# Kernel optimization log

Measured on AMD Instinct MI355X. Metric: run time of the kernel, lower is better.

The kernel has to match this reference:

```python
import jax, jax.numpy as jnp
import numpy as np

V, D, L, H, FF, B, S = 32000, 2048, 4, 16, 8192, 2, 2048
DH = D // H
PRUNE_LAYERS = (1, 2)   # layers with an attached pruning module
KEEP_RATIO = 0.5        # keep_ratio arg of forward_prefill_with_pruning


def _rms(x, w, eps=1e-6):
    return x * w * jax.lax.rsqrt(jnp.mean(x * x, -1, keepdims=True) + eps)


def _rope(x):
    # x: [B,H,s,DH]; position_ids = arange(s), recomputed after every pruning step
    s = x.shape[2]
    half = DH // 2
    inv = 1.0 / (10000.0 ** (jnp.arange(half, dtype=jnp.float32) / half))
    ang = jnp.arange(s, dtype=jnp.float32)[:, None] * inv  # [s, half]
    cos, sin = jnp.cos(ang), jnp.sin(ang)
    x1, x2 = x[..., :half], x[..., half:]
    return jnp.concatenate([x1 * cos - x2 * sin, x1 * sin + x2 * cos], -1)


def _block(h, mask, wq, wk, wv, wo, wg, wu, wd, ln1, ln2):
    b, s, _ = h.shape
    hn = _rms(h, ln1)
    q = _rope((hn @ wq).reshape(b, s, H, DH).transpose(0, 2, 1, 3))
    k = _rope((hn @ wk).reshape(b, s, H, DH).transpose(0, 2, 1, 3))
    v = (hn @ wv).reshape(b, s, H, DH).transpose(0, 2, 1, 3)
    att = jnp.einsum('bhqd,bhkd->bhqk', q, k) / np.float32(np.sqrt(DH))
    allowed = jnp.tril(jnp.ones((s, s), bool)) & (mask[:, None, None, :] > 0)
    att = jnp.where(allowed, att, jnp.float32(-1e9))
    o = jnp.einsum('bhqk,bhkd->bhqd', jax.nn.softmax(att, -1), v)
    h = h + o.transpose(0, 2, 1, 3).reshape(b, s, D) @ wo
    hn = _rms(h, ln2)
    h = h + (jax.nn.silu(hn @ wg) * (hn @ wu)) @ wd
    return h


def _forward(input_ids, attention_mask, embed, wq, wk, wv, wo, wg, wu, wd, ln1, ln2, lnf, lm_head, scorer):
    h = embed[input_ids]        # [B,S,D]
    mask = attention_mask
    for i in range(L):
        if i in PRUNE_LAYERS:
            pi = PRUNE_LAYERS.index(i)
            # pruning module: Linear(D->2); keep score = logits[..., 0]
            sc = jnp.einsum('bsd,cd->bsc', h, scorer[pi])[..., 0]
            kk = max(1, int(h.shape[1] * KEEP_RATIO))      # static under jit
            _, idx = jax.lax.top_k(sc, kk)
            idx = jnp.sort(idx, -1)                        # sorted kept indices
            h = jnp.take_along_axis(h, idx[..., None], axis=1)
            mask = jnp.take_along_axis(mask, idx, axis=1)
        h = _block(h, mask, wq[i], wk[i], wv[i], wo[i], wg[i], wu[i], wd[i], ln1[i], ln2[i])
    return _rms(h, lnf) @ lm_head   # logits [B, S_pruned, V]


def setup_inputs() -> dict:
    key = jax.random.key(0)
    ks = jax.random.split(key, 12)
    g = lambda k, shape: jax.random.normal(k, shape, jnp.float32) * 0.02
    return {
        'input_ids': jax.random.randint(ks[0], (B, S), 0, V, jnp.int32),
        'attention_mask': jnp.ones((B, S), jnp.int32),
        'embed': g(ks[1], (V, D)),
        'wq': g(ks[2], (L, D, D)),
        'wk': g(ks[3], (L, D, D)),
        'wv': g(ks[4], (L, D, D)),
        'wo': g(ks[5], (L, D, D)),
        'wg': g(ks[6], (L, D, FF)),
        'wu': g(ks[7], (L, D, FF)),
        'wd': g(ks[8], (L, FF, D)),
        'ln1': jnp.ones((L, D), jnp.float32),
        'ln2': jnp.ones((L, D), jnp.float32),
        'lnf': jnp.ones((D,), jnp.float32),
        'lm_head': g(ks[9], (D, V)),
        'scorer': g(ks[10], (len(PRUNE_LAYERS), 2, D)),
    }


def reference(input_ids, attention_mask, embed, wq, wk, wv, wo, wg, wu, wd, ln1, ln2, lnf, lm_head, scorer):
    return _forward(input_ids, attention_mask, embed, wq, wk, wv, wo, wg, wu, wd, ln1, ln2, lnf, lm_head, scorer)
```

## Files before the change

### kernel.cpp

```cpp
#include <hip/hip_runtime.h>
#include <math.h>


#define DD 2048
#define HH 16
#define DHH 128
#define FFF 8192
#define BBATCH 2
#define SSEQ 2048
#define VV 32000
#define LLAYERS 4

typedef float4 f4;
typedef __attribute__((ext_vector_type(8))) short short8;
typedef __attribute__((ext_vector_type(4))) float f32x4;
typedef unsigned short u16;

__device__ inline u16 bf16rne(float x) {
    unsigned u = __float_as_uint(x);
    unsigned r = (u + 0x7FFFu + ((u >> 16) & 1u)) >> 16;
    return (u16)r;
}
__device__ inline float bf16tof(u16 h) {
    return __uint_as_float(((unsigned)h) << 16);
}

__device__ __forceinline__ void gload16(const u16* g, u16* l) {
    __builtin_amdgcn_global_load_lds(
        (const __attribute__((address_space(1))) unsigned int*)g,
        (__attribute__((address_space(3))) unsigned int*)l, 16, 0, 0);
}

#define BARRIER() do { asm volatile("" ::: "memory"); \
    __builtin_amdgcn_s_barrier(); asm volatile("" ::: "memory"); } while (0)

__device__ __forceinline__ void xcd_swz(int& bx, int& by) {
    int gx = gridDim.x;
    int nwg = gx * gridDim.y;
    int orig = by * gx + bx;
    int q = nwg >> 3, r = nwg & 7;
    int xcd = orig & 7, loc = orig >> 3;
    int swz = (xcd < r ? xcd * (q + 1) : r * (q + 1) + (xcd - r) * q) + loc;
    bx = swz % gx;
    by = swz / gx;
}

__global__ void k_embed(const int* __restrict__ ids, const float* __restrict__ emb,
                        float* __restrict__ out) {
    int row = blockIdx.x;
    int id  = ids[row];
    const f4* src = (const f4*)(emb + (size_t)id * DD);
    f4*       dst = (f4*)(out + (size_t)row * DD);
    for (int i = threadIdx.x; i < DD / 4; i += blockDim.x) dst[i] = src[i];
}

__global__ void k_copy_int(const int* __restrict__ src, int* __restrict__ dst, int n) {
    int i = blockIdx.x * blockDim.x + threadIdx.x;
    if (i < n) dst[i] = src[i];
}

__global__ void k_addN(float* __restrict__ H, const float* __restrict__ P,
                       long len, int nparts) {
    long i = (long)blockIdx.x * 256 + threadIdx.x;
    if (i >= len / 4) return;
    f4 h = ((f4*)H)[i];
    for (int z = 0; z < nparts; z++) {
        f4 p = ((const f4*)(P + (size_t)z * len))[i];
        h.x += p.x; h.y += p.y; h.z += p.z; h.w += p.w;
    }
    ((f4*)H)[i] = h;
}

__global__ __launch_bounds__(256) void k_rmsnorm_cvt(const float* __restrict__ x,
                                                     const float* __restrict__ w,
                                                     u16* __restrict__ OH,
                                                     u16* __restrict__ OL) {
    int row = blockIdx.x;
    const float* xr = x + (size_t)row * DD;
    float ss = 0.f;
    for (int i = threadIdx.x; i < DD / 4; i += blockDim.x) {
        f4 v = ((const f4*)xr)[i];
        ss += v.x * v.x + v.y * v.y + v.z * v.z + v.w * v.w;
    }
    for (int o = 32; o > 0; o >>= 1) ss += __shfl_down(ss, o);
    __shared__ float red[4];
    int wid = threadIdx.x >> 6, lane = threadIdx.x & 63;
    if (lane == 0) red[wid] = ss;
    __syncthreads();
    float tot = red[0] + red[1] + red[2] + red[3];
    float inv = 1.0f / sqrtf(tot / (float)DD + 1e-6f);
    for (int i = threadIdx.x; i < DD / 4; i += blockDim.x) {
        f4 v = ((const f4*)xr)[i];
        f4 wv = ((const f4*)w)[i];
        float o[4];
        o[0] = v.x * wv.x * inv; o[1] = v.y * wv.y * inv;
        o[2] = v.z * wv.z * inv; o[3] = v.w * wv.w * inv;
        ushort4 hv, lv;
        u16* hp = (u16*)&hv; u16* lp = (u16*)&lv;
#pragma unroll
        for (int j = 0; j < 4; j++) {
            u16 h = bf16rne(o[j]);
            hp[j] = h;
            lp[j] = bf16rne(o[j] - bf16tof(h));
        }
        *(ushort4*)&OH[(size_t)row * DD + i * 4] = hv;
        *(ushort4*)&OL[(size_t)row * DD + i * 4] = lv;
    }
}

__global__ __launch_bounds__(256) void k_cvt_w(const float* __restrict__ W,
                                               u16* __restrict__ WtH,
                                               u16* __restrict__ WtL,
                                               int K, int N, int nc0, int dn0,
                                               int writeLo) {
    __shared__ float T[64][65];
    int tid = threadIdx.x;
    int n0g = nc0 + blockIdx.x * 64;
    int k0  = blockIdx.y * 64;
#pragma unroll
    for (int it = 0; it < 4; it++) {
        int r = it * 16 + (tid >> 4);
        int c4 = (tid & 15) * 4;
        f4 v = *(const f4*)(W + (size_t)(k0 + r) * N + n0g + c4);
        T[r][c4 + 0] = v.x; T[r][c4 + 1] = v.y;
        T[r][c4 + 2] = v.z; T[r][c4 + 3] = v.w;
    }
    __syncthreads();
    int nl = tid >> 2;
    int ks = (tid & 3) * 16;
    u16 hi[16], lo[16];
#pragma unroll
    for (int j = 0; j < 16; j++) {
        float v = T[ks + j][nl];
        u16 h = bf16rne(v);
        hi[j] = h;
        lo[j] = bf16rne(v - bf16tof(h));
    }
    size_t base = (size_t)(dn0 + blockIdx.x * 64 + nl) * K + k0 + ks;
    *(short8*)&WtH[base]     = *(short8*)&hi[0];
    *(short8*)&WtH[base + 8] = *(short8*)&hi[8];
    if (writeLo) {
        *(short8*)&WtL[base]     = *(short8*)&lo[0];
        *(short8*)&WtL[base + 8] = *(short8*)&lo[8];
    }
}

template <int PASSES, int RES, int DUAL>
__global__ __launch_bounds__(256, 2) void k_bgemm(const u16* __restrict__ AH,
                                                  const u16* __restrict__ AL,
                                                  const u16* __restrict__ B1H,
                                                  const u16* __restrict__ B1L,
                                                  const u16* __restrict__ B2H,
                                                  const u16* __restrict__ B2L,
                                                  const float* __restrict__ Rsrc,
                                                  float* __restrict__ C,
                                                  u16* __restrict__ OH,
                                                  u16* __restrict__ OL,
                                                  int M, int ldC, int K) {
    constexpr int NW = DUAL ? 2 : 1;
    __shared__ u16 As[128 * 32];
    __shared__ u16 Bs[NW][128 * 32];
    int tid = threadIdx.x;
    int bx = blockIdx.x, by = blockIdx.y;
    xcd_swz(bx, by);
    int m0 = by * 128, n0 = bx * 128;
    int lane = tid & 63, w = tid >> 6;
    int wm = w >> 1, wn = w & 1;
    int lr = lane & 15, lq = lane >> 4;
    int grow = lane >> 2;
    int gcol = (lane & 3) * 8;

    f32x4 acc[NW][4][4];
#pragma unroll
    for (int u = 0; u < NW; u++)
#pragma unroll
        for (int i = 0; i < 4; i++)
#pragma unroll
            for (int j = 0; j < 4; j++)
#pragma unroll
                for (int r = 0; r < 4; r++) acc[u][i][j][r] = 0.f;

    const int KT = PASSES * K;
    for (int kb = 0; kb < KT; kb += 32) {
        int p  = (PASSES > 1) ? ((kb >= 2 * K) ? 2 : ((kb >= K) ? 1 : 0)) : 0;
        int ks = kb - p * K;
        const u16* Ab = ((p == 2) ? AL  : AH)  + (size_t)(m0 + w * 32) * K + ks;
        const u16* Bb = ((p == 1) ? B1L : B1H) + (size_t)(n0 + w * 32) * K + ks;
        __syncthreads();
        gload16(Ab + (size_t)grow * K + gcol,        &As[w * 1024]);
        gload16(Ab + (size_t)(grow + 16) * K + gcol, &As[w * 1024 + 512]);
        gload16(Bb + (size_t)grow * K + gcol,        &Bs[0][w * 1024]);
        gload16(Bb + (size_t)(grow + 16) * K + gcol, &Bs[0][w * 1024 + 512]);
        if constexpr (DUAL) {
            const u16* B2b = ((p == 1) ? B2L : B2H) + (size_t)(n0 + w * 32) * K + ks;
            gload16(B2b + (size_t)grow * K + gcol,        &Bs[1][w * 1024]);
            gload16(B2b + (size_t)(grow + 16) * K + gcol, &Bs[1][w * 1024 + 512]);
        }
// ... 184 lines not shown
    }

#pragma unroll
    for (int i16 = 0; i16 < 8; i16++) {
#pragma unroll
        for (int jj = 0; jj < 4; jj++) {
            int gm = m0 + (i16 >> 2) * 128 + wm * 64 + (i16 & 3) * 16 + lq * 4;
            int gn = n0 + (jj >> 1) * 128 + wn * 32 + (jj & 1) * 16 + lr;
#pragma unroll
            for (int r = 0; r < 4; r++) {
                size_t off = (size_t)(gm + r) * ldC + gn;
                float v = acc[i16][jj][r];
                if constexpr (PLANE) {
                    u16 h = bf16rne(v);
                    OH[off] = h;
                    OL[off] = bf16rne(v - bf16tof(h));
                } else {
                    C[off] = v;
                }
            }
        }
    }
}

__global__ __launch_bounds__(256) void k_silu_cvt(const u16* __restrict__ Gh,
                                                  const u16* __restrict__ Gl,
                                                  u16* __restrict__ FH,
                                                  u16* __restrict__ FL, long n8) {
    long i = (long)blockIdx.x * 256 + threadIdx.x;
    if (i >= n8) return;
    short8 gh = ((const short8*)Gh)[i], gl = ((const short8*)Gl)[i];
    short8 uh = ((const short8*)FH)[i], ul = ((const short8*)FL)[i];
    short8 oh, ol;
#pragma unroll
    for (int e = 0; e < 8; e++) {
        float g = bf16tof((u16)gh[e]) + bf16tof((u16)gl[e]);
        float u = bf16tof((u16)uh[e]) + bf16tof((u16)ul[e]);
        float v = g / (1.0f + expf(-g)) * u;
        u16 h = bf16rne(v);
        oh[e] = (short)h;
        ol[e] = (short)bf16rne(v - bf16tof(h));
    }
    ((short8*)FH)[i] = oh;
    ((short8*)FL)[i] = ol;
}

__global__ void k_rope_table(float* __restrict__ cosT, float* __restrict__ sinT) {
    int idx = blockIdx.x * blockDim.x + threadIdx.x;
    if (idx >= SSEQ * 64) return;
    int pos = idx >> 6, d = idx & 63;
    float p   = (float)pow(10000.0, (double)d * (1.0 / 64.0));
    float inv = 1.0f / p;
    float ang = (float)pos * inv;
    cosT[idx] = (float)cos((double)ang);
    sinT[idx] = (float)sin((double)ang);
}

__global__ void k_rope(float* __restrict__ C,
                       const float* __restrict__ cosT, const float* __restrict__ sinT,
                       int s, int ld) {
    int bi = blockIdx.x;
    int h = bi % HH;
    int i = (bi / HH) % s;
    size_t base = (size_t)(bi / HH) * ld + h * DHH;
    int d = threadIdx.x;
    float c  = cosT[i * 64 + d];
    float sn = sinT[i * 64 + d];
    float x1 = C[base + d], x2 = C[base + 64 + d];
    C[base + d]      = x1 * c - x2 * sn;
    C[base + 64 + d] = x1 * sn + x2 * c;
    x1 = C[base + 2048 + d]; x2 = C[base + 2048 + 64 + d];
    C[base + 2048 + d]      = x1 * c - x2 * sn;
    C[base + 2048 + 64 + d] = x1 * sn + x2 * c;
}

__global__ __launch_bounds__(256) void k_cvt_qk(const float* __restrict__ C,
                                                u16* __restrict__ QHp, u16* __restrict__ QLp,
                                                u16* __restrict__ KHp, u16* __restrict__ KLp) {
    int row = blockIdx.x;
    int c = threadIdx.x * 8;
#pragma unroll
    for (int sec = 0; sec < 2; sec++) {
        const float* src = C + (size_t)row * 6144 + sec * 2048 + c;
        u16* dh = (sec ? KHp : QHp) + (size_t)row * 2048 + c;
        u16* dl = (sec ? KLp : QLp) + (size_t)row * 2048 + c;
        u16 hbuf[8], lbuf[8];
#pragma unroll
        for (int q = 0; q < 2; q++) {
            f4 v = *(const f4*)(src + q * 4);
            float a[4] = {v.x, v.y, v.z, v.w};
#pragma unroll
            for (int e = 0; e < 4; e++) {
                u16 h = bf16rne(a[e]);
                hbuf[q * 4 + e] = h;
                lbuf[q * 4 + e] = bf16rne(a[e] - bf16tof(h));
            }
        }
        *(short8*)dh = *(short8*)&hbuf[0];
        *(short8*)dl = *(short8*)&lbuf[0];
    }
}

__global__ __launch_bounds__(256) void k_cvt_vt(const float* __restrict__ C,
                                                u16* __restrict__ VtH,
                                                u16* __restrict__ VtL, int s) {
    __shared__ float T[64][132];
    int bh = blockIdx.y;
    int h = bh & 15, b = bh >> 4;
    int kv0 = blockIdx.x * 64;
    int t = threadIdx.x;
#pragma unroll
    for (int it = 0; it < 8; it++) {
        int kv = it * 8 + (t >> 5);
        int c4 = (t & 31) * 4;
        f4 v = *(const f4*)(C + (size_t)((size_t)b * s + kv0 + kv) * 6144 + 4096 + h * 128 + c4);
        T[kv][c4 + 0] = v.x; T[kv][c4 + 1] = v.y;
        T[kv][c4 + 2] = v.z; T[kv][c4 + 3] = v.w;
    }
    __syncthreads();
    int d = t >> 1, seg = t & 1;
    size_t base = ((size_t)bh * 128 + d) * s + kv0 + seg * 32;
#pragma unroll
    for (int g = 0; g < 4; g++) {
        u16 h8[8], l8[8];
#pragma unroll
        for (int e = 0; e < 8; e++) {
            float v = T[seg * 32 + g * 8 + e][d];
            u16 hh = bf16rne(v);
            h8[e] = hh;
            l8[e] = bf16rne(v - bf16tof(hh));
        }
        int gp = (g ^ ((d >> 1) & 3)) * 8;
        *(short8*)&VtH[base + gp] = *(short8*)&h8[0];
        *(short8*)&VtL[base + gp] = *(short8*)&l8[0];
    }
}

template <int PASSES>
__global__ __launch_bounds__(256, 2) void k_attn_mfma(
        const u16* __restrict__ QHp, const u16* __restrict__ QLp,
        const u16* __restrict__ KHp, const u16* __restrict__ KLp,
        const u16* __restrict__ VtH, const u16* __restrict__ VtL,
        const int* __restrict__ mask,
        u16* __restrict__ OH, u16* __restrict__ OL, int s) {
    constexpr int BUFU = (PASSES > 1) ? 16384 : 8192;
    constexpr int VOFF = (PASSES > 1) ? 8192 : 4096;
    __shared__ u16 SM[2 * BUFU + 5120];
    int tid = threadIdx.x, lane = tid & 63, w = tid >> 6;
    int lr = lane & 15, lq = lane >> 4;
    int grow = lane >> 2;
    int sgcol = (((lane & 3) ^ ((lane >> 3) & 3))) * 8;
    int gcol  = (lane & 3) * 8;
    int rc = (lq ^ ((lr >> 1) & 3)) * 8;
    int qt = gridDim.x - 1 - blockIdx.x;
    int bh = blockIdx.y;
    int h = bh & 15, b = bh >> 4;
    int q0 = qt * 64;
    size_t rb = (size_t)b * s;
    const u16* vtH = VtH + (size_t)bh * 128 * s;
    const u16* vtL = VtL + (size_t)bh * 128 * s;
    u16* PHw = SM + 2 * BUFU + w * 1280;
    u16* PLw = PHw + 640;
    const float scale = 0.08838834764831845f;

    short8 qh[4], ql[4];
    {
        const u16* qp = QHp + (rb + q0) * 2048 + h * 128 + w * 32;
#pragma unroll
        for (int it = 0; it < 4; it++)
            gload16(qp + (size_t)(it * 16 + grow) * 2048 + sgcol, SM + w * 2048 + it * 512);
        __syncthreads();
#pragma unroll
        for (int ks = 0; ks < 4; ks++)
            qh[ks] = *(const short8*)&SM[ks * 2048 + (w * 16 + lr) * 32 + rc];
        if constexpr (PASSES > 1) {
            __syncthreads();
            const u16* qp2 = QLp + (rb + q0) * 2048 + h * 128 + w * 32;
#pragma unroll
            for (int it = 0; it < 4; it++)
                gload16(qp2 + (size_t)(it * 16 + grow) * 2048 + sgcol, SM + w * 2048 + it * 512);
            __syncthreads();
#pragma unroll
            for (int ks = 0; ks < 4; ks++)
                ql[ks] = *(const short8*)&SM[ks * 2048 + (w * 16 + lr) * 32 + rc];
        }
        __syncthreads();
    }

    auto kv_stage = [&](int t, int buf) {
        u16* base = SM + buf * BUFU;
        const u16* kp = KHp + (rb + t * 32) * 2048 + h * 128 + w * 32;
        gload16(kp + (size_t)grow * 2048 + sgcol,        base + w * 1024);
        gload16(kp + (size_t)(16 + grow) * 2048 + sgcol, base + w * 1024 + 512);
        const u16* vp = vtH + (size_t)(w * 32) * s + t * 32;
        gload16(vp + (size_t)grow * s + gcol,        base + VOFF + (w * 32) * 32);
        gload16(vp + (size_t)(16 + grow) * s + gcol, base + VOFF + (w * 32 + 16) * 32);
        if constexpr (PASSES > 1) {
            const u16* kp2 = KLp + (rb + t * 32) * 2048 + h * 128 + w * 32;
            gload16(kp2 + (size_t)grow * 2048 + sgcol,        base + 4096 + w * 1024);
            gload16(kp2 + (size_t)(16 + grow) * 2048 + sgcol, base + 4096 + w * 1024 + 512);
            const u16* vp2 = vtL + (size_t)(w * 32) * s + t * 32;
            gload16(vp2 + (size_t)grow * s + gcol,        base + 12288 + (w * 32) * 32);
            gload16(vp2 + (size_t)(16 + grow) * s + gcol, base + 12288 + (w * 32 + 16) * 32);
        }
    };

    f32x4 o_acc[8];
#pragma unroll
    for (int j = 0; j < 8; j++)
#pragma unroll
        for (int r = 0; r < 4; r++) o_acc[j][r] = 0.f;
    float m_run[4], l_run[4];
#pragma unroll
    for (int r = 0; r < 4; r++) { m_run[r] = -3.0e38f; l_run[r] = 0.f; }

    int nt = (q0 + 64) >> 5;
    int mv0 = mask[rb + lr];
    int mv1 = mask[rb + 16 + lr];
    kv_stage(0, 0);
    for (int t = 0; t < nt; t++) {
        int bsel = t & 1;
        if (t + 1 < nt) {
            kv_stage(t + 1, 1 - bsel);
            if constexpr (PASSES > 1)
                asm volatile("s_waitcnt vmcnt(8)" ::: "memory");
            else
                asm volatile("s_waitcnt vmcnt(4)" ::: "memory");
        } else {
            asm volatile("s_waitcnt vmcnt(0)" ::: "memory");
        }
        BARRIER();
        int nmv0 = mv0, nmv1 = mv1;
        if (t + 1 < nt) {
            nmv0 = mask[rb + (t + 1) * 32 + lr];
            nmv1 = mask[rb + (t + 1) * 32 + 16 + lr];
        }
        const u16* KsH = SM + bsel * BUFU;
        const u16* KsL = KsH + 4096;
        const u16* VsH = SM + bsel * BUFU + VOFF;
        const u16* VsL = SM + bsel * BUFU + 12288;
        f32x4 sa[2];
#pragma unroll
        for (int j = 0; j < 2; j++)
#pragma unroll
            for (int r = 0; r < 4; r++) sa[j][r] = 0.f;
#pragma unroll
        for (int j = 0; j < 2; j++) {
#pragma unroll
            for (int ks = 0; ks < 4; ks++) {
                short8 kb = *(const short8*)&KsH[ks * 1024 + (j * 16 + lr) * 32 + rc];
                sa[j] = __builtin_amdgcn_mfma_f32_16x16x32_bf16(qh[ks], kb, sa[j], 0, 0, 0);
                if constexpr (PASSES > 1) {
                    short8 kl2 = *(const short8*)&KsL[ks * 1024 + (j * 16 + lr) * 32 + rc];
                    sa[j] = __builtin_amdgcn_mfma_f32_16x16x32_bf16(qh[ks], kl2, sa[j], 0, 0, 0);
                    sa[j] = __builtin_amdgcn_mfma_f32_16x16x32_bf16(ql[ks], kb, sa[j], 0, 0, 0);
                }
            }
        }
        float sclv[4];
#pragma unroll
        for (int r = 0; r < 4; r++) {
            int ig = q0 + w * 16 + lq * 4 + r;
            float v0 = (t * 32 + lr <= ig && mv0 > 0) ? sa[0][r] * scale : -1.0e9f;
            float v1 = (t * 32 + 16 + lr <= ig && mv1 > 0) ? sa[1][r] * scale : -1.0e9f;
            float mx = fmaxf(v0, v1);
            mx = fmaxf(mx, __shfl_xor(mx, 1));
            mx = fmaxf(mx, __shfl_xor(mx, 2));
            mx = fmaxf(mx, __shfl_xor(mx, 4));
            mx = fmaxf(mx, __shfl_xor(mx, 8));
            float mo = m_run[r];
            float mn = fmaxf(mo, mx);
            float p0 = expf(v0 - mn), p1 = expf(v1 - mn);
            float ps = p0 + p1;
            ps += __shfl_xor(ps, 1);
            ps += __shfl_xor(ps, 2);
            ps += __shfl_xor(ps, 4);
            ps += __shfl_xor(ps, 8);
            sclv[r] = expf(mo - mn);
            m_run[r] = mn;
            l_run[r] = l_run[r] * sclv[r] + ps;
            int prow = lq * 4 + r;
            u16 h0 = bf16rne(p0);
            u16 h1 = bf16rne(p1);
            PHw[prow * 40 + lr] = h0;
            PHw[prow * 40 + 16 + lr] = h1;
            if constexpr (PASSES > 1) {
                PLw[prow * 40 + lr] = bf16rne(p0 - bf16tof(h0));
                PLw[prow * 40 + 16 + lr] = bf16rne(p1 - bf16tof(h1));
            }
        }
#pragma unroll
        for (int j = 0; j < 8; j++)
#pragma unroll
            for (int r = 0; r < 4; r++) o_acc[j][r] *= sclv[r];
        short8 ph = *(const short8*)&PHw[lr * 40 + lq * 8];
        short8 pl;
        if constexpr (PASSES > 1) pl = *(const short8*)&PLw[lr * 40 + lq * 8];
#pragma unroll
        for (int j = 0; j < 8; j++) {
            int vrow = j * 16 + lr;
            short8 vh = *(const short8*)&VsH[vrow * 32 + rc];
            o_acc[j] = __builtin_amdgcn_mfma_f32_16x16x32_bf16(ph, vh, o_acc[j], 0, 0, 0);
            if constexpr (PASSES > 1) {
                short8 vl = *(const short8*)&VsL[vrow * 32 + rc];
                o_acc[j] = __builtin_amdgcn_mfma_f32_16x16x32_bf16(ph, vl, o_acc[j], 0, 0, 0);
                o_acc[j] = __builtin_amdgcn_mfma_f32_16x16x32_bf16(pl, vh, o_acc[j], 0, 0, 0);
            }
        }
        BARRIER();
        mv0 = nmv0; mv1 = nmv1;
    }
#pragma unroll
    for (int r = 0; r < 4; r++) {
        float linv = 1.0f / l_run[r];
        size_t rowoff = (rb + q0 + w * 16 + lq * 4 + r) * 2048 + h * 128 + lr;
#pragma unroll
        for (int j = 0; j < 8; j++) {
            float v = o_acc[j][r] * linv;
            u16 hh = bf16rne(v);
            OH[rowoff + j * 16] = hh;
            OL[rowoff + j * 16] = bf16rne(v - bf16tof(hh));
        }
    }
}

__global__ __launch_bounds__(256, 2) void k_attn_f32(const float* __restrict__ Q,
                                                     const float* __restrict__ K,
                                                     const float* __restrict__ V,
                                                     const int* __restrict__ mask,
                                                     u16* __restrict__ OH,
                                                     u16* __restrict__ OL, int s, int ld) {
    int qt = blockIdx.x, bh = blockIdx.y;
    int h = bh & (HH - 1), b = bh >> 4;
    __shared__ float Qs[64][132];
    __shared__ float Ks[32 * 128];
    __shared__ float Vs[32][132];
    __shared__ float Ps[64][36];
    __shared__ float mrow[64], lrow[64];
    int tid = threadIdx.x;
    int tx = tid & 15, ty = tid >> 4;

#pragma unroll
    for (int p = 0; p < 2; p++) {
        int r = p * 32 + (tid >> 3);
        int kb = (tid & 7) * 4;
        const float* src = Q + (size_t)(b * s + qt * 64 + r) * ld + h * DHH;
#pragma unroll
        for (int q = 0; q < 4; q++)
            *(f4*)&Qs[r][kb + 32 * q] = *(const f4*)(src + kb + 32 * q);
    }
    if (tid < 64) { mrow[tid] = -3.0e38f; lrow[tid] = 0.f; }

    float acc[4][8];
#pragma unroll
    for (int i = 0; i < 4; i++)
#pragma unroll
        for (int c = 0; c < 8; c++) acc[i][c] = 0.f;
    const float scale = 0.08838834764831845f;

    int ktmax = 2 * (qt + 1);
    for (int kt = 0; kt < ktmax; kt++) {
        __syncthreads();
#pragma unroll
        for (int p = 0; p < 4; p++) {
            int c = p * 8 + (tid >> 5);
            int kk = (tid & 31) * 4;
            size_t g = (size_t)(b * s + kt * 32 + c) * ld + h * DHH + kk;
            f4 kv = *(const f4*)(K + g);
            int ch = (kk >> 2) ^ (c >> 1);
            *(f4*)&Ks[c * 128 + ch * 4] = kv;
            *(f4*)&Vs[c][kk] = *(const f4*)(V + g);
        }
        __syncthreads();
        float sv[4][2];
#pragma unroll
        for (int i = 0; i < 4; i++) { sv[i][0] = 0.f; sv[i][1] = 0.f; }
        for (int kk = 0; kk < 128; kk += 4) {
            f4 qv[4];
#pragma unroll
            for (int i = 0; i < 4; i++) qv[i] = *(const f4*)&Qs[ty * 4 + i][kk];
#pragma unroll
            for (int j = 0; j < 2; j++) {
                int c = tx * 2 + j;
                int ch = (kk >> 2) ^ (c >> 1);
                f4 kv = *(const f4*)&Ks[c * 128 + ch * 4];
#pragma unroll
                for (int i = 0; i < 4; i++)
                    sv[i][j] += qv[i].x * kv.x + qv[i].y * kv.y +
                                qv[i].z * kv.z + qv[i].w * kv.w;
            }
        }
        float scl[4];
#pragma unroll
        for (int i = 0; i < 4; i++) {
            int r = ty * 4 + i;
            int igl = qt * 64 + r;
#pragma unroll
            for (int j = 0; j < 2; j++) {
                int jg = kt * 32 + tx * 2 + j;
                bool ok = (jg <= igl) && (mask[b * s + jg] > 0);
                sv[i][j] = ok ? sv[i][j] * scale : -1.0e9f;
            }
            float rmax = fmaxf(sv[i][0], sv[i][1]);
            rmax = fmaxf(rmax, __shfl_xor(rmax, 1));
            rmax = fmaxf(rmax, __shfl_xor(rmax, 2));
            rmax = fmaxf(rmax, __shfl_xor(rmax, 4));
            rmax = fmaxf(rmax, __shfl_xor(rmax, 8));
            float mold = mrow[r];
            float mnew = fmaxf(mold, rmax);
            float p0 = expf(sv[i][0] - mnew);
            float p1 = expf(sv[i][1] - mnew);
            float ps = p0 + p1;
            ps += __shfl_xor(ps, 1);
            ps += __shfl_xor(ps, 2);
            ps += __shfl_xor(ps, 4);
            ps += __shfl_xor(ps, 8);
            scl[i] = expf(mold - mnew);
            if (tx == 0) { mrow[r] = mnew; lrow[r] = lrow[r] * scl[i] + ps; }
            float2 pw; pw.x = p0; pw.y = p1;
            *(float2*)&Ps[r][tx * 2] = pw;
        }
        __syncthreads();
#pragma unroll
        for (int i = 0; i < 4; i++) {
            float sc = scl[i];
#pragma unroll
            for (int c = 0; c < 8; c++) acc[i][c] *= sc;
        }
        for (int jj = 0; jj < 32; jj += 4) {
            f4 pv[4];
#pragma unroll
            for (int i = 0; i < 4; i++) pv[i] = *(const f4*)&Ps[ty * 4 + i][jj];
#pragma unroll
            for (int j2 = 0; j2 < 4; j2++) {
                f4 va = *(const f4*)&Vs[jj + j2][tx * 4];
                f4 vb = *(const f4*)&Vs[jj + j2][64 + tx * 4];
#pragma unroll
                for (int i = 0; i < 4; i++) {
                    float p = (&pv[i].x)[j2];
                    acc[i][0] += p * va.x; acc[i][1] += p * va.y;
                    acc[i][2] += p * va.z; acc[i][3] += p * va.w;
                    acc[i][4] += p * vb.x; acc[i][5] += p * vb.y;
                    acc[i][6] += p * vb.z; acc[i][7] += p * vb.w;
                }
            }
        }
    }
    __syncthreads();
#pragma unroll
    for (int i = 0; i < 4; i++) {
        int r = ty * 4 + i;
        float linv = 1.0f / lrow[r];
        size_t ob = (size_t)(b * s + qt * 64 + r) * DD + h * DHH;
        ushort4 h1, l1, h2, l2;
        u16 *h1p = (u16*)&h1, *l1p = (u16*)&l1, *h2p = (u16*)&h2, *l2p = (u16*)&l2;
#pragma unroll
        for (int c = 0; c < 4; c++) {
            float v = acc[i][c] * linv;
            u16 hh = bf16rne(v);
            h1p[c] = hh; l1p[c] = bf16rne(v - bf16tof(hh));
            float v2 = acc[i][c + 4] * linv;
            u16 hh2 = bf16rne(v2);
            h2p[c] = hh2; l2p[c] = bf16rne(v2 - bf16tof(hh2));
        }
        *(ushort4*)&OH[ob + tx * 4] = h1;
        *(ushort4*)&OL[ob + tx * 4] = l1;
        *(ushort4*)&OH[ob + 64 + tx * 4] = h2;
        *(ushort4*)&OL[ob + 64 + tx * 4] = l2;
    }
}

__global__ __launch_bounds__(256) void k_score(const float* __restrict__ Hb,
                                               const float* __restrict__ srow,
                                               float* __restrict__ sc) {
// ... 41 lines not shown
}

__global__ void k_gather(const float* __restrict__ Hin, const int* __restrict__ idx,
                         float* __restrict__ Hout, int s, int kk) {
    int row = blockIdx.x;
    int b = row / kk, p = row % kk;
    int i = idx[b * kk + p];
    const f4* src = (const f4*)(Hin + (size_t)(b * s + i) * DD);
    f4* dst = (f4*)(Hout + (size_t)row * DD);
    for (int t = threadIdx.x; t < DD / 4; t += blockDim.x) dst[t] = src[t];
}

__global__ void k_gather_mask(const int* __restrict__ Min, const int* __restrict__ idx,
                              int* __restrict__ Mout, int s, int kk) {
    int t = blockIdx.x * blockDim.x + threadIdx.x;
    if (t < BBATCH * kk) {
        int b = t / kk, p = t % kk;
        Mout[t] = Min[b * s + idx[b * kk + p]];
    }
}

extern "C" void kernel_launch(void* const* d_in, const int* in_sizes, int n_in,
                              void* d_out, int out_size, void* d_ws, size_t ws_size,
                              hipStream_t stream) {
    const int*   input_ids = (const int*)d_in[0];
    const int*   attn_mask = (const int*)d_in[1];
    const float* embed     = (const float*)d_in[2];
    const float* wq        = (const float*)d_in[3];
    const float* wk        = (const float*)d_in[4];
    const float* wv        = (const float*)d_in[5];
    const float* wo        = (const float*)d_in[6];
    const float* wg        = (const float*)d_in[7];
    const float* wu        = (const float*)d_in[8];
    const float* wd        = (const float*)d_in[9];
    const float* ln1       = (const float*)d_in[10];
    const float* ln2       = (const float*)d_in[11];
    const float* lnf       = (const float*)d_in[12];
    const float* lm_head   = (const float*)d_in[13];
    const float* scorer    = (const float*)d_in[14];

    float* ws = (float*)d_ws;
    const size_t R = (size_t)BBATCH * SSEQ * DD;
    const size_t MISC_FLOATS = 2 * SSEQ * 64 + 5 * (size_t)BBATCH * SSEQ + 1024;
    const size_t NEED_A = (14 * R + MISC_FLOATS) * 4;
    const bool bigws = (ws_size >= NEED_A);

    float* H0   = ws;
    float* H1   = ws + R;
    float* CQKV = ws + 2 * R;
    u16*   AH   = (u16*)(ws + 5 * R);
    u16*   AL   = AH + (size_t)4096 * DD;

    u16* QHp = (u16*)(ws + 6 * R);
    u16* QLp = QHp + (size_t)4096 * DD;
    u16* KHp = (u16*)(ws + 7 * R);
    u16* KLp = KHp + (size_t)4096 * DD;
    u16* VtH = (u16*)(ws + 8 * R);
    u16* VtL = VtH + (size_t)4096 * DD;
    u16* FH  = (u16*)(ws + 6 * R);
    u16* FL  = (u16*)(ws + 8 * R);
    u16* WH1 = (u16*)(ws + 10 * R);
    u16* WL1 = WH1 + (size_t)FFF * DD;
    u16* WH2 = (u16*)(ws + 12 * R);
    u16* WL2 = WH2 + (size_t)FFF * DD;
    u16* WDH = (u16*)(ws + 10 * R);
    u16* WDL = WDH + (size_t)DD * FFF;
    u16* WQKVH = (u16*)(ws + 10 * R);
    u16* WQKVL = WQKVH + (size_t)6144 * DD;

    u16* cWgH = (u16*)CQKV;
    u16* cWgL = cWgH + (size_t)2048 * DD;
    u16* cWuH = cWgL + (size_t)2048 * DD;
    u16* cWuL = cWuH + (size_t)2048 * DD;
    u16* cFH  = (u16*)(ws + 3 * R);
    u16* cFL  = cFH + (size_t)4096 * 2048;
    u16* cWdH = (u16*)(ws + 4 * R);
    u16* cWdL = cWdH + (size_t)2048 * DD;

    float* miscB = ws + (bigws ? 14 * R : 6 * R);
    float* COS = miscB;
    float* SIN = COS + SSEQ * 64;
    float* SC  = SIN + SSEQ * 64;
    int*   FLG = (int*)(SC + (size_t)BBATCH * SSEQ);
    int*   IDX = FLG + BBATCH * SSEQ;
    int*   M0  = IDX + BBATCH * SSEQ;
    int*   M1  = M0 + BBATCH * SSEQ;

    k_rope_table<<<(SSEQ * 64 + 255) / 256, 256, 0, stream>>>(COS, SIN);
    k_embed<<<BBATCH * SSEQ, 256, 0, stream>>>(input_ids, embed, H0);
    k_copy_int<<<(BBATCH * SSEQ + 255) / 256, 256, 0, stream>>>(attn_mask, M0, BBATCH * SSEQ);

    float* Hc = H0; float* Nc = H1;
    int*   Mc = M0; int*   Mt = M1;
    int s = SSEQ;

    for (int l = 0; l < LLAYERS; l++) {
        if (l == 1 || l == 2) {
            int pi = l - 1;
            int kk = s / 2;
            k_score<<<BBATCH * s, 256, 0, stream>>>(Hc, scorer + (size_t)pi * 2 * DD, SC);
            k_rank<<<BBATCH * s, 256, 0, stream>>>(SC, FLG, s, kk);
            k_compact<<<BBATCH, 64, 0, stream>>>(FLG, IDX, s, kk);
            k_gather<<<BBATCH * kk, 256, 0, stream>>>(Hc, IDX, Nc, s, kk);
            k_gather_mask<<<(BBATCH * kk + 255) / 256, 256, 0, stream>>>(Mc, IDX, Mt, s, kk);
            { float* t = Hc; Hc = Nc; Nc = t; }
            { int* t = Mc; Mc = Mt; Mt = t; }
            s = kk;
        }
        int rows = BBATCH * s;
        const bool hiP = (l < 2);
        const int wlo = hiP ? 1 : 0;
        const float* Wq = wq + (size_t)l * DD * DD;
        const float* Wk = wk + (size_t)l * DD * DD;
        const float* Wv = wv + (size_t)l * DD * DD;
        const float* Wo = wo + (size_t)l * DD * DD;
        const float* Wg = wg + (size_t)l * DD * FFF;
        const float* Wu = wu + (size_t)l * DD * FFF;
        const float* Wd = wd + (size_t)l * FFF * DD;
        const float* L1 = ln1 + (size_t)l * DD;
        const float* L2 = ln2 + (size_t)l * DD;

        dim3 gWd(DD / 64, DD / 64);

        k_rmsnorm_cvt<<<rows, 256, 0, stream>>>(Hc, L1, AH, AL);
        if (bigws) {
            k_cvt_w<<<gWd, 256, 0, stream>>>(Wq, WQKVH, WQKVL, DD, DD, 0, 0, wlo);
            k_cvt_w<<<gWd, 256, 0, stream>>>(Wk, WQKVH, WQKVL, DD, DD, 0, 2048, wlo);
            k_cvt_w<<<gWd, 256, 0, stream>>>(Wv, WQKVH, WQKVL, DD, DD, 0, 4096, wlo);
            if (rows >= 2048) {
                dim3 gQKV(6144 / 256, rows / 256);
                if (hiP) k_bg256<3,0><<<gQKV,512,0,stream>>>(AH,AL,WQKVH,WQKVL,CQKV,nullptr,nullptr,rows,6144,DD,DD);
                else     k_bg256<1,0><<<gQKV,512,0,stream>>>(AH,AL,WQKVH,WQKVL,CQKV,nullptr,nullptr,rows,6144,DD,DD);
            } else {
                dim3 gQKV(6144 / 128, rows / 128);
                k_bgemm<1,0,0><<<gQKV,256,0,stream>>>(AH,AL,WQKVH,WQKVL,nullptr,nullptr,nullptr,CQKV,nullptr,nullptr,rows,6144,DD);
            }
        } else {
            u16* WtH = (u16*)Nc;
            u16* WtL = WtH + (size_t)DD * DD;
            dim3 gG(DD / 128, rows / 128);
            const float* Wqkv[3] = {Wq, Wk, Wv};
            for (int q3 = 0; q3 < 3; q3++) {
                k_cvt_w<<<gWd, 256, 0, stream>>>(Wqkv[q3], WtH, WtL, DD, DD, 0, 0, wlo);
                float* Cb = CQKV + q3 * 2048;
                if (hiP) k_bgemm<3,0,0><<<gG,256,0,stream>>>(AH,AL,WtH,WtL,nullptr,nullptr,nullptr,Cb,nullptr,nullptr,rows,6144,DD);
                else     k_bgemm<1,0,0><<<gG,256,0,stream>>>(AH,AL,WtH,WtL,nullptr,nullptr,nullptr,Cb,nullptr,nullptr,rows,6144,DD);
            }
        }
        k_rope<<<rows * HH, 64, 0, stream>>>(CQKV, COS, SIN, s, 6144);

        if (bigws) {
            k_cvt_qk<<<rows, 256, 0, stream>>>(CQKV, QHp, QLp, KHp, KLp);
            k_cvt_vt<<<dim3(s / 64, BBATCH * HH), 256, 0, stream>>>(CQKV, VtH, VtL, s);
            if (hiP) k_attn_mfma<3><<<dim3(s / 64, BBATCH * HH), 256, 0, stream>>>(
                         QHp, QLp, KHp, KLp, VtH, VtL, Mc, AH, AL, s);
            else     k_attn_mfma<1><<<dim3(s / 64, BBATCH * HH), 256, 0, stream>>>(
                         QHp, QLp, KHp, KLp, VtH, VtL, Mc, AH, AL, s);
        } else {
            k_attn_f32<<<dim3(s / 64, BBATCH * HH), 256, 0, stream>>>(
                CQKV, CQKV + 2048, CQKV + 4096, Mc, AH, AL, s, 6144);
        }

        {
            u16* WtH = bigws ? WQKVH : (u16*)Nc;
            u16* WtL = bigws ? (WQKVH + (size_t)DD * DD) : ((u16*)Nc + (size_t)DD * DD);
            k_cvt_w<<<gWd, 256, 0, stream>>>(Wo, WtH, WtL, DD, DD, 0, 0, wlo);
            if (bigws && hiP) {
                int SK = (rows >= 4096) ? 2 : 4;
                float* P = ws + 2 * R;
                dim3 g(DD / 256, rows / 256, SK);
                k_bg256<3,0><<<g, 512, 0, stream>>>(AH, AL, WtH, WtL, P,
                                                    nullptr, nullptr, rows, DD, DD / SK, DD);
                long len = (long)rows * DD;
                k_addN<<<(len / 4 + 255) / 256, 256, 0, stream>>>(Hc, P, len, SK);
            } else {
                dim3 gG(DD / 128, rows / 128);
                if (hiP) k_bgemm<3,1,0><<<gG,256,0,stream>>>(AH,AL,WtH,WtL,nullptr,nullptr,Hc,Hc,nullptr,nullptr,rows,DD,DD);
                else     k_bgemm<1,1,0><<<gG,256,0,stream>>>(AH,AL,WtH,WtL,nullptr,nullptr,Hc,Hc,nullptr,nullptr,rows,DD,DD);
            }
        }

        k_rmsnorm_cvt<<<rows, 256, 0, stream>>>(Hc, L2, AH, AL);
        if (bigws && rows >= 2048) {
            k_cvt_w<<<dim3(FFF / 64, DD / 64), 256, 0, stream>>>(Wg, WH1, WL1, DD, FFF, 0, 0, wlo);
            k_cvt_w<<<dim3(FFF / 64, DD / 64), 256, 0, stream>>>(Wu, WH2, WL2, DD, FFF, 0, 0, wlo);
            u16* Gh = (l == 0) ? (u16*)(ws + R) : (u16*)(ws + 2 * R);
            u16* Gl = (u16*)(ws + 3 * R);
            dim3 gMLP(FFF / 256, rows / 256);
            if (hiP) {
                k_bg256<3,1><<<gMLP,512,0,stream>>>(AH,AL,WH1,WL1,nullptr,Gh,Gl,rows,FFF,DD,DD);
                k_bg256<3,1><<<gMLP,512,0,stream>>>(AH,AL,WH2,WL2,nullptr,FH,FL,rows,FFF,DD,DD);
            } else {
                k_bg256<1,1><<<gMLP,512,0,stream>>>(AH,AL,WH1,WL1,nullptr,Gh,Gl,rows,FFF,DD,DD);
                k_bg256<1,1><<<gMLP,512,0,stream>>>(AH,AL,WH2,WL2,nullptr,FH,FL,rows,FFF,DD,DD);
            }
            long n8 = (long)rows * FFF / 8;
            k_silu_cvt<<<(n8 + 255) / 256, 256, 0, stream>>>(Gh, Gl, FH, FL, n8);
            k_cvt_w<<<dim3(DD / 64, FFF / 64), 256, 0, stream>>>(Wd, WDH, WDL, FFF, DD, 0, 0, wlo);
            int SK = (rows >= 4096) ? 2 : 4;
            float* P = ws + 2 * R;
            dim3 gD(DD / 256, rows / 256, SK);
            if (hiP) k_bg256<3,0><<<gD,512,0,stream>>>(FH,FL,WDH,WDL,P,nullptr,nullptr,rows,DD,FFF/SK,FFF);
            else     k_bg256<1,0><<<gD,512,0,stream>>>(FH,FL,WDH,WDL,P,nullptr,nullptr,rows,DD,FFF/SK,FFF);
            long len = (long)rows * DD;
            k_addN<<<(len / 4 + 255) / 256, 256, 0, stream>>>(Hc, P, len, SK);
        } else if (bigws) {
            k_cvt_w<<<dim3(FFF / 64, DD / 64), 256, 0, stream>>>(Wg, WH1, WL1, DD, FFF, 0, 0, wlo);
            k_cvt_w<<<dim3(FFF / 64, DD / 64), 256, 0, stream>>>(Wu, WH2, WL2, DD, FFF, 0, 0, wlo);
            k_bgemm<1,0,1><<<dim3(FFF/128, rows/128),256,0,stream>>>(AH,AL,WH1,WL1,WH2,WL2,nullptr,nullptr,FH,FL,rows,FFF,DD);
            k_cvt_w<<<dim3(DD / 64, FFF / 64), 256, 0, stream>>>(Wd, WDH, WDL, FFF, DD, 0, 0, wlo);
            k_bgemm<1,1,0><<<dim3(DD/128, rows/128),256,0,stream>>>(FH,FL,WDH,WDL,nullptr,nullptr,Hc,Hc,nullptr,nullptr,rows,DD,FFF);
        } else {
            for (int ffc = 0; ffc < FFF; ffc += 2048) {
                k_cvt_w<<<dim3(2048 / 64, DD / 64), 256, 0, stream>>>(Wg, cWgH, cWgL, DD, FFF, ffc, 0, wlo);
                k_cvt_w<<<dim3(2048 / 64, DD / 64), 256, 0, stream>>>(Wu, cWuH, cWuL, DD, FFF, ffc, 0, wlo);
                if (hiP) k_bgemm<3,0,1><<<dim3(16, rows/128),256,0,stream>>>(AH,AL,cWgH,cWgL,cWuH,cWuL,nullptr,nullptr,cFH,cFL,rows,2048,DD);
                else     k_bgemm<1,0,1><<<dim3(16, rows/128),256,0,stream>>>(AH,AL,cWgH,cWgL,cWuH,cWuL,nullptr,nullptr,cFH,cFL,rows,2048,DD);
                k_cvt_w<<<dim3(DD / 64, 2048 / 64), 256, 0, stream>>>(Wd + (size_t)ffc * DD, cWdH, cWdL, 2048, DD, 0, 0, wlo);
                if (hiP) k_bgemm<3,1,0><<<dim3(DD/128, rows/128),256,0,stream>>>(cFH,cFL,cWdH,cWdL,nullptr,nullptr,Hc,Hc,nullptr,nullptr,rows,DD,2048);
                else     k_bgemm<1,1,0><<<dim3(DD/128, rows/128),256,0,stream>>>(cFH,cFL,cWdH,cWdL,nullptr,nullptr,Hc,Hc,nullptr,nullptr,rows,DD,2048);
            }
        }
    }

    int rows = BBATCH * s;
    u16* AHf = (u16*)Nc;
    u16* ALf = AHf + (size_t)rows * DD;
    u16* LmH = bigws ? (u16*)(ws + 6 * R) : (u16*)CQKV;
    k_rmsnorm_cvt<<<rows, 256, 0, stream>>>(Hc, lnf, AHf, ALf);
    k_cvt_w<<<dim3(VV / 64, DD / 64), 256, 0, stream>>>(lm_head, LmH, LmH, DD, VV, 0, 0, 0);
    if (bigws) {
        k_bg256<1, 0><<<dim3(VV / 256, rows / 256), 512, 0, stream>>>(
            AHf, ALf, LmH, LmH, (float*)d_out, nullptr, nullptr, rows, VV, DD, DD);
    } else {
        k_bgemm<1,0,0><<<dim3(VV / 128, rows / 128), 256, 0, stream>>>(
            AHf, ALf, LmH, LmH, nullptr, nullptr, nullptr, (float*)d_out,
            nullptr, nullptr, rows, VV, DD);
    }
}
```

Measured before the change: 4.740 ms.

## Process two 64-row query subtiles per attention block and XCD-swizzle block order

The MFMA flash-attention kernel now handles 128 query rows per block as two 64-row subtiles that share each staged K/V tile, halving the grid and the K/V global-to-LDS traffic per query row. Subtiles lying entirely above the causal diagonal skip work for that K tile. Block indices are remapped with an XCD-aware swizzle so blocks of the same head land on the same XCD. The generic xcd_swz helper also changes to a column-major ordering. The cost is doubled accumulator and register state per wave, which may reduce occupancy or cause spills, plus coarser load balance across causal tiles.

```diff
diff --git a/kernel.cpp b/kernel.cpp
--- a/kernel.cpp
+++ b/kernel.cpp
@@ -35,14 +35,14 @@
     __builtin_amdgcn_s_barrier(); asm volatile("" ::: "memory"); } while (0)
 
 __device__ __forceinline__ void xcd_swz(int& bx, int& by) {
-    int gx = gridDim.x;
-    int nwg = gx * gridDim.y;
-    int orig = by * gx + bx;
+    int gy = gridDim.y;
+    int nwg = gridDim.x * gy;
+    int orig = bx * gy + by;
     int q = nwg >> 3, r = nwg & 7;
     int xcd = orig & 7, loc = orig >> 3;
     int swz = (xcd < r ? xcd * (q + 1) : r * (q + 1) + (xcd - r) * q) + loc;
-    bx = swz % gx;
-    by = swz / gx;
+    bx = swz / gy;
+    by = swz % gy;
 }
 
 __global__ void k_embed(const int* __restrict__ ids, const float* __restrict__ emb,
@@ -533,10 +533,16 @@
     int sgcol = (((lane & 3) ^ ((lane >> 3) & 3))) * 8;
     int gcol  = (lane & 3) * 8;
     int rc = (lq ^ ((lr >> 1) & 3)) * 8;
-    int qt = gridDim.x - 1 - blockIdx.x;
-    int bh = blockIdx.y;
+    int gx = gridDim.x;
+    int NB = gx * gridDim.y;
+    int orig = blockIdx.y * gx + blockIdx.x;
+    int qq = NB >> 3, rr = NB & 7;
+    int xcd = orig & 7, loc = orig >> 3;
+    int swz = (xcd < rr ? xcd * (qq + 1) : rr * (qq + 1) + (xcd - rr) * qq) + loc;
+    int bh = swz / gx;
+    int qt = gx - 1 - (swz % gx);
     int h = bh & 15, b = bh >> 4;
-    int q0 = qt * 64;
+    int q0 = qt * 128;
     size_t rb = (size_t)b * s;
     const u16* vtH = VtH + (size_t)bh * 128 * s;
     const u16* vtL = VtL + (size_t)bh * 128 * s;
@@ -544,26 +550,27 @@
     u16* PLw = PHw + 640;
     const float scale = 0.08838834764831845f;
 
-    short8 qh[4], ql[4];
-    {
-        const u16* qp = QHp + (rb + q0) * 2048 + h * 128 + w * 32;
+    short8 qh[2][4], ql[2][4];
+#pragma unroll
+    for (int st = 0; st < 2; st++) {
+        const u16* qp = QHp + (rb + q0 + st * 64) * 2048 + h * 128 + w * 32;
 #pragma unroll
         for (int it = 0; it < 4; it++)
             gload16(qp + (size_t)(it * 16 + grow) * 2048 + sgcol, SM + w * 2048 + it * 512);
         __syncthreads();
 #pragma unroll
         for (int ks = 0; ks < 4; ks++)
-            qh[ks] = *(const short8*)&SM[ks * 2048 + (w * 16 + lr) * 32 + rc];
+            qh[st][ks] = *(const short8*)&SM[ks * 2048 + (w * 16 + lr) * 32 + rc];
         if constexpr (PASSES > 1) {
             __syncthreads();
-            const u16* qp2 = QLp + (rb + q0) * 2048 + h * 128 + w * 32;
+            const u16* qp2 = QLp + (rb + q0 + st * 64) * 2048 + h * 128 + w * 32;
 #pragma unroll
             for (int it = 0; it < 4; it++)
                 gload16(qp2 + (size_t)(it * 16 + grow) * 2048 + sgcol, SM + w * 2048 + it * 512);
             __syncthreads();
 #pragma unroll
             for (int ks = 0; ks < 4; ks++)
-                ql[ks] = *(const short8*)&SM[ks * 2048 + (w * 16 + lr) * 32 + rc];
+                ql[st][ks] = *(const short8*)&SM[ks * 2048 + (w * 16 + lr) * 32 + rc];
         }
         __syncthreads();
     }
@@ -586,16 +593,20 @@
         }
     };
 
-    f32x4 o_acc[8];
-#pragma unroll
-    for (int j = 0; j < 8; j++)
-#pragma unroll
-        for (int r = 0; r < 4; r++) o_acc[j][r] = 0.f;
-    float m_run[4], l_run[4];
-#pragma unroll
-    for (int r = 0; r < 4; r++) { m_run[r] = -3.0e38f; l_run[r] = 0.f; }
-
-    int nt = (q0 + 64) >> 5;
+    f32x4 o_acc[2][8];
+#pragma unroll
+    for (int st = 0; st < 2; st++)
+#pragma unroll
+        for (int j = 0; j < 8; j++)
+#pragma unroll
+            for (int r = 0; r < 4; r++) o_acc[st][j][r] = 0.f;
+    float m_run[2][4], l_run[2][4];
+#pragma unroll
+    for (int st = 0; st < 2; st++)
+#pragma unroll
+        for (int r = 0; r < 4; r++) { m_run[st][r] = -3.0e38f; l_run[st][r] = 0.f; }
+
+    int nt = (q0 + 128) >> 5;
     int mv0 = mask[rb + lr];
     int mv1 = mask[rb + 16 + lr];
     kv_stage(0, 0);
@@ -620,87 +631,94 @@
         const u16* KsL = KsH + 4096;
         const u16* VsH = SM + bsel * BUFU + VOFF;
         const u16* VsL = SM + bsel * BUFU + 12288;
-        f32x4 sa[2];
-#pragma unroll
-        for (int j = 0; j < 2; j++)
-#pragma unroll
-            for (int r = 0; r < 4; r++) sa[j][r] = 0.f;
-#pragma unroll
-        for (int j = 0; j < 2; j++) {
-#pragma unroll
-            for (int ks = 0; ks < 4; ks++) {
-                short8 kb = *(const short8*)&KsH[ks * 1024 + (j * 16 + lr) * 32 + rc];
-                sa[j] = __builtin_amdgcn_mfma_f32_16x16x32_bf16(qh[ks], kb, sa[j], 0, 0, 0);
+#pragma unroll
+        for (int st = 0; st < 2; st++) {
+            if (t * 32 > q0 + st * 64 + w * 16 + 15) continue;
+            f32x4 sa[2];
+#pragma unroll
+            for (int j = 0; j < 2; j++)
+#pragma unroll
+                for (int r = 0; r < 4; r++) sa[j][r] = 0.f;
+#pragma unroll
+            for (int j = 0; j < 2; j++) {
+#pragma unroll
+                for (int ks = 0; ks < 4; ks++) {
+                    short8 kb = *(const short8*)&KsH[ks * 1024 + (j * 16 + lr) * 32 + rc];
+                    sa[j] = __builtin_amdgcn_mfma_f32_16x16x32_bf16(qh[st][ks], kb, sa[j], 0, 0, 0);
+                    if constexpr (PASSES > 1) {
+                        short8 kl2 = *(const short8*)&KsL[ks * 1024 + (j * 16 + lr) * 32 + rc];
+                        sa[j] = __builtin_amdgcn_mfma_f32_16x16x32_bf16(qh[st][ks], kl2, sa[j], 0, 0, 0);
+                        sa[j] = __builtin_amdgcn_mfma_f32_16x16x32_bf16(ql[st][ks], kb, sa[j], 0, 0, 0);
+                    }
+                }
+            }
+            float sclv[4];
+#pragma unroll
+            for (int r = 0; r < 4; r++) {
+                int ig = q0 + st * 64 + w * 16 + lq * 4 + r;
+                float v0 = (t * 32 + lr <= ig && mv0 > 0) ? sa[0][r] * scale : -1.0e9f;
+                float v1 = (t * 32 + 16 + lr <= ig && mv1 > 0) ? sa[1][r] * scale : -1.0e9f;
+                float mx = fmaxf(v0, v1);
+                mx = fmaxf(mx, __shfl_xor(mx, 1));
+                mx = fmaxf(mx, __shfl_xor(mx, 2));
+                mx = fmaxf(mx, __shfl_xor(mx, 4));
+                mx = fmaxf(mx, __shfl_xor(mx, 8));
+                float mo = m_run[st][r];
+                float mn = fmaxf(mo, mx);
+                float p0 = expf(v0 - mn), p1 = expf(v1 - mn);
+                float ps = p0 + p1;
+                ps += __shfl_xor(ps, 1);
+                ps += __shfl_xor(ps, 2);
+                ps += __shfl_xor(ps, 4);
+                ps += __shfl_xor(ps, 8);
+                sclv[r] = expf(mo - mn);
+                m_run[st][r] = mn;
+                l_run[st][r] = l_run[st][r] * sclv[r] + ps;
+                int prow = lq * 4 + r;
+                u16 h0 = bf16rne(p0);
+                u16 h1 = bf16rne(p1);
+                PHw[prow * 40 + lr] = h0;
+                PHw[prow * 40 + 16 + lr] = h1;
                 if constexpr (PASSES > 1) {
-                    short8 kl2 = *(const short8*)&KsL[ks * 1024 + (j * 16 + lr) * 32 + rc];
-                    sa[j] = __builtin_amdgcn_mfma_f32_16x16x32_bf16(qh[ks], kl2, sa[j], 0, 0, 0);
-                    sa[j] = __builtin_amdgcn_mfma_f32_16x16x32_bf16(ql[ks], kb, sa[j], 0, 0, 0);
+                    PLw[prow * 40 + lr] = bf16rne(p0 - bf16tof(h0));
+                    PLw[prow * 40 + 16 + lr] = bf16rne(p1 - bf16tof(h1));
                 }
             }
-        }
-        float sclv[4];
-#pragma unroll
-        for (int r = 0; r < 4; r++) {
-            int ig = q0 + w * 16 + lq * 4 + r;
-            float v0 = (t * 32 + lr <= ig && mv0 > 0) ? sa[0][r] * scale : -1.0e9f;
-            float v1 = (t * 32 + 16 + lr <= ig && mv1 > 0) ? sa[1][r] * scale : -1.0e9f;
-            float mx = fmaxf(v0, v1);
-            mx = fmaxf(mx, __shfl_xor(mx, 1));
-            mx = fmaxf(mx, __shfl_xor(mx, 2));
-            mx = fmaxf(mx, __shfl_xor(mx, 4));
-            mx = fmaxf(mx, __shfl_xor(mx, 8));
-            float mo = m_run[r];
-            float mn = fmaxf(mo, mx);
-            float p0 = expf(v0 - mn), p1 = expf(v1 - mn);
-            float ps = p0 + p1;
-            ps += __shfl_xor(ps, 1);
-            ps += __shfl_xor(ps, 2);
-            ps += __shfl_xor(ps, 4);
-            ps += __shfl_xor(ps, 8);
-            sclv[r] = expf(mo - mn);
-            m_run[r] = mn;
-            l_run[r] = l_run[r] * sclv[r] + ps;
-            int prow = lq * 4 + r;
-            u16 h0 = bf16rne(p0);
-            u16 h1 = bf16rne(p1);
-            PHw[prow * 40 + lr] = h0;
-            PHw[prow * 40 + 16 + lr] = h1;
-            if constexpr (PASSES > 1) {
-                PLw[prow * 40 + lr] = bf16rne(p0 - bf16tof(h0));
-                PLw[prow * 40 + 16 + lr] = bf16rne(p1 - bf16tof(h1));
-            }
-        }
-#pragma unroll
-        for (int j = 0; j < 8; j++)
-#pragma unroll
-            for (int r = 0; r < 4; r++) o_acc[j][r] *= sclv[r];
-        short8 ph = *(const short8*)&PHw[lr * 40 + lq * 8];
-        short8 pl;
-        if constexpr (PASSES > 1) pl = *(const short8*)&PLw[lr * 40 + lq * 8];
-#pragma unroll
-        for (int j = 0; j < 8; j++) {
-            int vrow = j * 16 + lr;
-            short8 vh = *(const short8*)&VsH[vrow * 32 + rc];
-            o_acc[j] = __builtin_amdgcn_mfma_f32_16x16x32_bf16(ph, vh, o_acc[j], 0, 0, 0);
-            if constexpr (PASSES > 1) {
-                short8 vl = *(const short8*)&VsL[vrow * 32 + rc];
-                o_acc[j] = __builtin_amdgcn_mfma_f32_16x16x32_bf16(ph, vl, o_acc[j], 0, 0, 0);
-                o_acc[j] = __builtin_amdgcn_mfma_f32_16x16x32_bf16(pl, vh, o_acc[j], 0, 0, 0);
+#pragma unroll
+            for (int j = 0; j < 8; j++)
+#pragma unroll
+                for (int r = 0; r < 4; r++) o_acc[st][j][r] *= sclv[r];
+            short8 ph = *(const short8*)&PHw[lr * 40 + lq * 8];
+            short8 pl;
+            if constexpr (PASSES > 1) pl = *(const short8*)&PLw[lr * 40 + lq * 8];
+#pragma unroll
+            for (int j = 0; j < 8; j++) {
+                int vrow = j * 16 + lr;
+                short8 vh = *(const short8*)&VsH[vrow * 32 + rc];
+                o_acc[st][j] = __builtin_amdgcn_mfma_f32_16x16x32_bf16(ph, vh, o_acc[st][j], 0, 0, 0);
+                if constexpr (PASSES > 1) {
+                    short8 vl = *(const short8*)&VsL[vrow * 32 + rc];
+                    o_acc[st][j] = __builtin_amdgcn_mfma_f32_16x16x32_bf16(ph, vl, o_acc[st][j], 0, 0, 0);
+                    o_acc[st][j] = __builtin_amdgcn_mfma_f32_16x16x32_bf16(pl, vh, o_acc[st][j], 0, 0, 0);
+                }
             }
         }
         BARRIER();
         mv0 = nmv0; mv1 = nmv1;
     }
 #pragma unroll
-    for (int r = 0; r < 4; r++) {
-        float linv = 1.0f / l_run[r];
-        size_t rowoff = (rb + q0 + w * 16 + lq * 4 + r) * 2048 + h * 128 + lr;
-#pragma unroll
-        for (int j = 0; j < 8; j++) {
-            float v = o_acc[j][r] * linv;
-            u16 hh = bf16rne(v);
-            OH[rowoff + j * 16] = hh;
-            OL[rowoff + j * 16] = bf16rne(v - bf16tof(hh));
+    for (int st = 0; st < 2; st++) {
+#pragma unroll
+        for (int r = 0; r < 4; r++) {
+            float linv = 1.0f / l_run[st][r];
+            size_t rowoff = (rb + q0 + st * 64 + w * 16 + lq * 4 + r) * 2048 + h * 128 + lr;
+#pragma unroll
+            for (int j = 0; j < 8; j++) {
+                float v = o_acc[st][j][r] * linv;
+                u16 hh = bf16rne(v);
+                OH[rowoff + j * 16] = hh;
+                OL[rowoff + j * 16] = bf16rne(v - bf16tof(hh));
+            }
         }
     }
 }
@@ -1048,9 +1066,9 @@
         if (bigws) {
             k_cvt_qk<<<rows, 256, 0, stream>>>(CQKV, QHp, QLp, KHp, KLp);
             k_cvt_vt<<<dim3(s / 64, BBATCH * HH), 256, 0, stream>>>(CQKV, VtH, VtL, s);
-            if (hiP) k_attn_mfma<3><<<dim3(s / 64, BBATCH * HH), 256, 0, stream>>>(
+            if (hiP) k_attn_mfma<3><<<dim3(s / 128, BBATCH * HH), 256, 0, stream>>>(
                          QHp, QLp, KHp, KLp, VtH, VtL, Mc, AH, AL, s);
-            else     k_attn_mfma<1><<<dim3(s / 64, BBATCH * HH), 256, 0, stream>>>(
+            else     k_attn_mfma<1><<<dim3(s / 128, BBATCH * HH), 256, 0, stream>>>(
                          QHp, QLp, KHp, KLp, VtH, VtL, Mc, AH, AL, s);
         } else {
             k_attn_f32<<<dim3(s / 64, BBATCH * HH), 256, 0, stream>>>(
```

Result: no change. 4.773 ms (+0.7%).
